# Kernel tuning notes

Measured on AMD Instinct MI355X. Metric: run time of the kernel, lower is better.

The kernel has to match this reference:

```python
import jax, jax.numpy as jnp
import numpy as np

U = 100000   # num_users
I = 50000    # num_items
N = U + I    # total nodes
D = 64       # embed_size
L = 3        # n_layers
E = 2000000  # num edges
EPS = 1e-12  # F.normalize default eps


def setup_inputs() -> dict:
    key = jax.random.key(0)
    k1, k2, k3, k4 = jax.random.split(key, 4)
    user_emb = jax.random.normal(k1, (U, D), dtype=jnp.float32) * 0.1
    item_emb = jax.random.normal(k2, (I, D), dtype=jnp.float32) * 0.1
    rows = jax.random.randint(k3, (E,), 0, N, dtype=jnp.int32)
    cols = jax.random.randint(k4, (E,), 0, N, dtype=jnp.int32)
    return {"user_emb": user_emb, "item_emb": item_emb, "rows": rows, "cols": cols}


def _spmm(vals, rows, cols, x):
    # sparse [N,N] @ dense [N,D] via gather + segment reduce
    return jax.ops.segment_sum(vals[:, None] * x[cols], rows, num_segments=N)


def _l2norm(x):
    return x / jnp.maximum(jnp.linalg.norm(x, axis=1, keepdims=True), EPS)


def reference(user_emb, item_emb, rows, cols):
    emb0 = jnp.concatenate([user_emb, item_emb], axis=0)  # [N, D]

    # laplacian_adj: G = D^-1/2 A D^-1/2 on the same edge set
    deg = jax.ops.segment_sum(jnp.ones((E,), emb0.dtype), rows, num_segments=N)
    d_is = jnp.where(deg > 0, deg ** -0.5, 0.0)
    g_vals = d_is[rows] * d_is[cols]  # [E]

    cur = emb0
    acc = emb0
    user_fine, item_fine = [], []
    for _ in range(L):
        gnn = _spmm(g_vals, rows, cols, cur)  # [N, D]
        # fine_laplacian_adj: cosine-sim edge scores, row-normalized
        gr = _l2norm(gnn[rows])
        gc = _l2norm(gnn[cols])
        scores = (jnp.sum(gr * gc, axis=1) + 1.0) * 0.5  # [E] in [0,1]
        rowsum = jax.ops.segment_sum(scores, rows, num_segments=N)
        d_inv = jnp.where(rowsum > 0, 1.0 / rowsum, 0.0)
        fine = _spmm(d_inv[rows] * scores, rows, cols, cur)  # [N, D]
        cur = gnn + fine
        acc = acc + cur
        user_fine.append(fine[:U])
        item_fine.append(fine[U:])

    u_embs = acc[:U]
    i_embs = acc[U:]
    return (u_embs, i_embs, jnp.stack(user_fine, 0), jnp.stack(item_fine, 0))
```

## Files before the change

### kernel.cpp

```cpp
#include <hip/hip_runtime.h>

namespace {

typedef unsigned short u16;
typedef __attribute__((__ext_vector_type__(2))) float f32x2;
typedef __attribute__((__ext_vector_type__(4))) float f32x4;

constexpr int Un = 100000;
constexpr int In = 50000;
constexpr int Nn = 150000;
constexpr int D  = 64;
constexpr int Ln = 3;
constexpr int En = 2000000;
constexpr int CHUNK = 1024;
constexpr int NB = (Nn + CHUNK - 1) / CHUNK;
constexpr int DSTR = 8;

__device__ __forceinline__ u16 f2bf(float f) {
    unsigned u = __float_as_uint(f);
    unsigned r = (u + 0x7FFFu + ((u >> 16) & 1u)) >> 16;
    return (u16)r;
}
__device__ __forceinline__ float bflo(unsigned u) {
    return __uint_as_float(u << 16);
}
__device__ __forceinline__ float bfhi(unsigned u) {
    return __uint_as_float(u & 0xFFFF0000u);
}
__device__ __forceinline__ unsigned pack2(float lo, float hi) {
    return (unsigned)f2bf(lo) | ((unsigned)f2bf(hi) << 16);
}

__device__ __forceinline__ f32x2 pkfma(f32x2 a, f32x2 b, f32x2 c) {
    f32x2 d;
    asm("v_pk_fma_f32 %0, %1, %2, %3" : "=v"(d) : "v"(a), "v"(b), "v"(c));
    return d;
}
__device__ __forceinline__ f32x2 pkadd(f32x2 a, f32x2 b) {
    f32x2 d;
    asm("v_pk_add_f32 %0, %1, %2" : "=v"(d) : "v"(a), "v"(b));
    return d;
}

__device__ __forceinline__ float dpp_add8(float x) {
    x += __uint_as_float((unsigned)__builtin_amdgcn_update_dpp(
        0, (int)__float_as_uint(x), 0xB1, 0xF, 0xF, true));
    x += __uint_as_float((unsigned)__builtin_amdgcn_update_dpp(
        0, (int)__float_as_uint(x), 0x4E, 0xF, 0xF, true));
    x += __uint_as_float((unsigned)__builtin_amdgcn_update_dpp(
        0, (int)__float_as_uint(x), 0x141, 0xF, 0xF, true));
    return x;
}

__device__ __forceinline__ void unp8(uint4 q, f32x2* o) {
    o[0].x = bflo(q.x); o[0].y = bfhi(q.x);
    o[1].x = bflo(q.y); o[1].y = bfhi(q.y);
    o[2].x = bflo(q.z); o[2].y = bfhi(q.z);
    o[3].x = bflo(q.w); o[3].y = bfhi(q.w);
}

__global__ void count_kernel(const int* __restrict__ rows, int* __restrict__ deg8,
                             int* __restrict__ eoff) {
    int e = blockIdx.x * blockDim.x + threadIdx.x;
    if (e < En) eoff[e] = atomicAdd(&deg8[(size_t)rows[e] * DSTR], 1);
}

__global__ void scan_partial(const int* __restrict__ deg8, float* __restrict__ d_is,
                             int* __restrict__ bsum) {
    int tid = threadIdx.x;
    int base = blockIdx.x * CHUNK + tid * 4;
    int s = 0;
#pragma unroll
    for (int i = 0; i < 4; ++i) {
        int idx = base + i;
        if (idx < Nn) {
            int d = deg8[(size_t)idx * DSTR];
            s += d;
            d_is[idx] = d > 0 ? rsqrtf((float)d) : 0.f;
        }
    }
    __shared__ int sh[256];
    sh[tid] = s;
    __syncthreads();
    for (int o = 128; o > 0; o >>= 1) {
        if (tid < o) sh[tid] += sh[tid + o];
        __syncthreads();
    }
    if (tid == 0) bsum[blockIdx.x] = sh[0];
}

__global__ void scan_top(int* __restrict__ bsum, int* __restrict__ row_ptr) {
    __shared__ int sh[256];
    int tid = threadIdx.x;
    int v = (tid < NB) ? bsum[tid] : 0;
    sh[tid] = v;
    __syncthreads();
    for (int o = 1; o < 256; o <<= 1) {
        int t = (tid >= o) ? sh[tid - o] : 0;
        __syncthreads();
        sh[tid] += t;
        __syncthreads();
    }
    if (tid < NB) bsum[tid] = sh[tid] - v;
    if (tid == 255) row_ptr[Nn] = sh[255];
}

__global__ void scan_final(const int* __restrict__ deg8, const int* __restrict__ bsum,
                           int* __restrict__ row_ptr) {
    int tid = threadIdx.x;
    int base = blockIdx.x * CHUNK + tid * 4;
    int v[4];
    int ts = 0;
#pragma unroll
    for (int i = 0; i < 4; ++i) {
        int idx = base + i;
        v[i] = (idx < Nn) ? deg8[(size_t)idx * DSTR] : 0;
        ts += v[i];
    }
    __shared__ int sh[256];
    sh[tid] = ts;
    __syncthreads();
    for (int o = 1; o < 256; o <<= 1) {
        int t = (tid >= o) ? sh[tid - o] : 0;
        __syncthreads();
        sh[tid] += t;
        __syncthreads();
    }
    int excl = bsum[blockIdx.x] + sh[tid] - ts;
#pragma unroll
    for (int i = 0; i < 4; ++i) {
        int idx = base + i;
        if (idx < Nn) row_ptr[idx] = excl;
        excl += v[i];
    }
}

__global__ void fill_kernel(const int* __restrict__ rows, const int* __restrict__ cols,
                            const int* __restrict__ row_ptr, const int* __restrict__ eoff,
                            int* __restrict__ col_off) {
    int e = blockIdx.x * blockDim.x + threadIdx.x;
    if (e >= En) return;
    col_off[row_ptr[rows[e]] + eoff[e]] = cols[e] << 7;
}

__global__ void init_kernel(const float* __restrict__ ue, const float* __restrict__ ie,
                            const float* __restrict__ d_is,
                            u16* __restrict__ cur, u16* __restrict__ S) {
    int i8 = (blockIdx.x * 256 + threadIdx.x) * 8;
    if (i8 >= Nn * D) return;
    const float* src = (i8 < Un * D) ? (ue + i8) : (ie + (i8 - Un * D));
    float4 v0 = ((const float4*)src)[0];
    float4 v1 = ((const float4*)src)[1];
    uint4 qc;
    qc.x = pack2(v0.x, v0.y); qc.y = pack2(v0.z, v0.w);
    qc.z = pack2(v1.x, v1.y); qc.w = pack2(v1.z, v1.w);
    *(uint4*)((char*)cur + (size_t)i8 * 2) = qc;
    float ds = d_is[i8 >> 6];
    uint4 qs;
    qs.x = pack2(v0.x * ds, v0.y * ds); qs.y = pack2(v0.z * ds, v0.w * ds);
    qs.z = pack2(v1.x * ds, v1.y * ds); qs.w = pack2(v1.z * ds, v1.w * ds);
    *(uint4*)((char*)S + (size_t)i8 * 2) = qs;
}

__global__ __launch_bounds__(256) void spmm_gnn(const u16* __restrict__ S_,
                                                u16* __restrict__ Qn_,
                                                const int* __restrict__ row_ptr,
                                                const int* __restrict__ col_off,
                                                const float* __restrict__ d_is,
                                                float* __restrict__ normv) {
    int r = (blockIdx.x * 256 + threadIdx.x) >> 6;
    if (r >= Nn) return;
    int lane = threadIdx.x & 63;
    int g = lane >> 3, l = lane & 7;
    unsigned l16 = (unsigned)l * 16u;
    const char* pS = (const char*)S_;
    int s = row_ptr[r], t = row_ptr[r + 1];
    float dr = d_is[r];
    f32x2 z; z.x = 0.f; z.y = 0.f;
    f32x2 a2[4] = {z, z, z, z};
    int deg = t - s;
    int nfull = deg >> 3;
    int rem = deg & 7;
    int jb = s + g;
#pragma unroll 2
    for (int i = 0; i < nfull; ++i) {
        unsigned off = (unsigned)col_off[jb + i * 8];
        uint4 q = *(const uint4*)(pS + (off + l16));
        f32x2 x2[4];
        unp8(q, x2);
#pragma unroll
        for (int p = 0; p < 4; ++p) a2[p] = pkadd(a2[p], x2[p]);
    }
    if (g < rem) {
        unsigned off = (unsigned)col_off[jb + nfull * 8];
        uint4 q = *(const uint4*)(pS + (off + l16));
        f32x2 x2[4];
        unp8(q, x2);
#pragma unroll
        for (int p = 0; p < 4; ++p) a2[p] = pkadd(a2[p], x2[p]);
    }
    float a[8] = {a2[0].x, a2[0].y, a2[1].x, a2[1].y,
                  a2[2].x, a2[2].y, a2[3].x, a2[3].y};
#pragma unroll
    for (int k = 0; k < 8; ++k) {
        a[k] += __shfl_xor(a[k], 8);
        a[k] += __shfl_xor(a[k], 16);
        a[k] += __shfl_xor(a[k], 32);
    }
    float sq = 0.f;
#pragma unroll
    for (int k = 0; k < 8; ++k) sq = fmaf(a[k], a[k], sq);
    sq = dpp_add8(sq);
    float gn = dr * sqrtf(sq);
    float nrm = fmaxf(gn, 1e-12f);
    float scale = dr / nrm;
    if (lane == 8) normv[r] = nrm;
    if (g == 0) {
        unsigned ro = ((unsigned)r << 7) + l16;
        uint4 on;
        on.x = pack2(a[0] * scale, a[1] * scale);
        on.y = pack2(a[2] * scale, a[3] * scale);
        on.z = pack2(a[4] * scale, a[5] * scale);
        on.w = pack2(a[6] * scale, a[7] * scale);
        *(uint4*)((char*)Qn_ + ro) = on;
    }
}

__global__ __launch_bounds__(256) void score_fine_kernel(const u16* __restrict__ A_,
                                                         const u16* __restrict__ Qn_,
                                                         u16* __restrict__ C_,
                                                         u16* __restrict__ S_,
                                                         const float* __restrict__ normv,
                                                         const float* __restrict__ d_is,
                                                         const int* __restrict__ row_ptr,
                                                         const int* __restrict__ col_off,
                                                         float* __restrict__ out, int layer) {
    int r = (blockIdx.x * 256 + threadIdx.x) >> 6;
    if (r >= Nn) return;
    int lane = threadIdx.x & 63;
    int g = lane >> 3, l = lane & 7;
    unsigned l16 = (unsigned)l * 16u;
    const char* pQn = (const char*)Qn_;
    const char* pA  = (const char*)A_;
    int s = row_ptr[r], t = row_ptr[r + 1];
    float dsr = d_is[r];
    float nrm = normv[r];
    unsigned ro = ((unsigned)r << 7) + l16;
    uint4 qbn = *(const uint4*)(pQn + ro);
    f32x2 b2[4];
    unp8(qbn, b2);
    f32x2 z; z.x = 0.f; z.y = 0.f;
    f32x2 facc[4] = {z, z, z, z};
    float rowsum = 0.f;
    int deg = t - s;
    int nfull = deg >> 3;
    int rem = deg & 7;
    int jb = s + g;
#pragma unroll 2
    for (int i = 0; i < nfull; ++i) {
        unsigned off = (unsigned)col_off[jb + i * 8];
        unsigned vo = off + l16;
        uint4 qx = *(const uint4*)(pQn + vo);
        uint4 qy = *(const uint4*)(pA + vo);
        f32x2 x2[4];
        unp8(qx, x2);
        f32x2 d2 = pkfma(b2[0], x2[0], z);
        d2 = pkfma(b2[1], x2[1], d2);
        d2 = pkfma(b2[2], x2[2], d2);
        d2 = pkfma(b2[3], x2[3], d2);
        float d = dpp_add8(d2.x + d2.y);
        float sc = fmaf(d, 0.5f, 0.5f);
        rowsum += sc;
        f32x2 y2[4];
        unp8(qy, y2);
        f32x2 sc2; sc2.x = sc; sc2.y = sc;
#pragma unroll
        for (int p = 0; p < 4; ++p) facc[p] = pkfma(sc2, y2[p], facc[p]);
    }
    if (g < rem) {
        unsigned off = (unsigned)col_off[jb + nfull * 8];
        unsigned vo = off + l16;
        uint4 qx = *(const uint4*)(pQn + vo);
        uint4 qy = *(const uint4*)(pA + vo);
        f32x2 x2[4];
        unp8(qx, x2);
        f32x2 d2 = pkfma(b2[0], x2[0], z);
        d2 = pkfma(b2[1], x2[1], d2);
        d2 = pkfma(b2[2], x2[2], d2);
        d2 = pkfma(b2[3], x2[3], d2);
        float d = dpp_add8(d2.x + d2.y);
        float sc = fmaf(d, 0.5f, 0.5f);
        rowsum += sc;
        f32x2 y2[4];
        unp8(qy, y2);
        f32x2 sc2; sc2.x = sc; sc2.y = sc;
#pragma unroll
        for (int p = 0; p < 4; ++p) facc[p] = pkfma(sc2, y2[p], facc[p]);
    }
    float f[8] = {facc[0].x, facc[0].y, facc[1].x, facc[1].y,
                  facc[2].x, facc[2].y, facc[3].x, facc[3].y};
    rowsum += __shfl_xor(rowsum, 8);
    rowsum += __shfl_xor(rowsum, 16);
    rowsum += __shfl_xor(rowsum, 32);
#pragma unroll
    for (int k = 0; k < 8; ++k) {
        f[k] += __shfl_xor(f[k], 8);
        f[k] += __shfl_xor(f[k], 16);
        f[k] += __shfl_xor(f[k], 32);
    }
    float di = rowsum > 0.f ? 1.f / rowsum : 0.f;
#pragma unroll
    for (int k = 0; k < 8; ++k) f[k] *= di;
    float bb[8] = {b2[0].x, b2[0].y, b2[1].x, b2[1].y,
                   b2[2].x, b2[2].y, b2[3].x, b2[3].y};
    float cn[8];
#pragma unroll
    for (int k = 0; k < 8; ++k) cn[k] = fmaf(bb[k], nrm, f[k]);
    if (g == 0) {
        uint4 qn;
        qn.x = pack2(cn[0], cn[1]); qn.y = pack2(cn[2], cn[3]);
        qn.z = pack2(cn[4], cn[5]); qn.w = pack2(cn[6], cn[7]);
        *(uint4*)((char*)C_ + ro) = qn;
    }
    if (g == 1 && layer != Ln - 1) {
        uint4 qs;
        qs.x = pack2(cn[0] * dsr, cn[1] * dsr);
        qs.y = pack2(cn[2] * dsr, cn[3] * dsr);
        qs.z = pack2(cn[4] * dsr, cn[5] * dsr);
        qs.w = pack2(cn[6] * dsr, cn[7] * dsr);
        *(uint4*)((char*)S_ + ro) = qs;
    }
    if (g >= 2 && g <= 3) {
        size_t fo;
        if (r < Un)
            fo = (size_t)Nn * D + (size_t)layer * Un * D + (size_t)r * D + l * 8;
        else
            fo = (size_t)Nn * D + (size_t)Ln * Un * D + (size_t)layer * In * D
                 + (size_t)(r - Un) * D + l * 8;
        if (g == 2) {
            f32x4 f0; f0.x = f[0]; f0.y = f[1]; f0.z = f[2]; f0.w = f[3];
            __builtin_nontemporal_store(f0, (f32x4*)(out + fo));
        } else {
            f32x4 f1; f1.x = f[4]; f1.y = f[5]; f1.z = f[6]; f1.w = f[7];
            __builtin_nontemporal_store(f1, (f32x4*)(out + fo) + 1);
        }
    }
}

__global__ void final_sum(const float* __restrict__ ue, const float* __restrict__ ie,
                          const u16* __restrict__ c1, const u16* __restrict__ c2,
                          const u16* __restrict__ c3, float* __restrict__ out) {
    int i8 = (blockIdx.x * 256 + threadIdx.x) * 8;
    if (i8 >= Nn * D) return;
    const float* src = (i8 < Un * D) ? (ue + i8) : (ie + (i8 - Un * D));
    float4 v0 = ((const float4*)src)[0];
    float4 v1 = ((const float4*)src)[1];
    uint4 q1 = *(const uint4*)((const char*)c1 + (size_t)i8 * 2);
    uint4 q2 = *(const uint4*)((const char*)c2 + (size_t)i8 * 2);
    uint4 q3 = *(const uint4*)((const char*)c3 + (size_t)i8 * 2);
    float o[8] = {v0.x, v0.y, v0.z, v0.w, v1.x, v1.y, v1.z, v1.w};
    f32x2 t1[4], t2[4], t3[4];
    unp8(q1, t1); unp8(q2, t2); unp8(q3, t3);
#pragma unroll
    for (int p = 0; p < 4; ++p) {
        o[2 * p]     = ((o[2 * p]     + t1[p].x) + t2[p].x) + t3[p].x;
        o[2 * p + 1] = ((o[2 * p + 1] + t1[p].y) + t2[p].y) + t3[p].y;
    }
    float4 w0, w1;
    w0.x = o[0]; w0.y = o[1]; w0.z = o[2]; w0.w = o[3];
    w1.x = o[4]; w1.y = o[5]; w1.z = o[6]; w1.w = o[7];
    ((float4*)(out + i8))[0] = w0;
    ((float4*)(out + i8))[1] = w1;
}

}

extern "C" void kernel_launch(void* const* d_in, const int* in_sizes, int n_in,
                              void* d_out, int out_size, void* d_ws, size_t ws_size,
                              hipStream_t stream) {
    const float* user_emb = (const float*)d_in[0];
    const float* item_emb = (const float*)d_in[1];
    const int* rows = (const int*)d_in[2];
    const int* cols = (const int*)d_in[3];
    float* out = (float*)d_out;

    char* ws = (char*)d_ws;
    size_t off = 0;
    auto alloc = [&](size_t bytes) -> void* {
        void* p = ws + off;
        off += (bytes + 255) & ~size_t(255);
        return p;
    };
    u16*   bufA    = (u16*)  alloc((size_t)Nn * D * 2);
    u16*   bufB    = (u16*)  alloc((size_t)Nn * D * 2);
    u16*   bufC    = (u16*)  alloc((size_t)Nn * D * 2);
    u16*   Qn      = (u16*)  alloc((size_t)Nn * D * 2);
    u16*   S       = (u16*)  alloc((size_t)Nn * D * 2);
    int*   col_off = (int*)  alloc((size_t)(En + 8) * 4);
    int*   deg8    = (int*)  alloc((size_t)Nn * DSTR * 4);
    int*   row_ptr = (int*)  alloc((size_t)(Nn + 1) * 4);
    float* d_is    = (float*)alloc((size_t)Nn * 4);
    float* normv   = (float*)alloc((size_t)Nn * 4);
    int*   bsum    = (int*)  alloc(4096);
    int*   eoff    = (int*)Qn;
    (void)ws_size; (void)in_sizes; (void)n_in; (void)out_size;

    hipMemsetAsync(deg8, 0, (size_t)Nn * DSTR * 4, stream);

    const int EB = (En + 255) / 256;
    count_kernel<<<EB, 256, 0, stream>>>(rows, deg8, eoff);
    scan_partial<<<NB, 256, 0, stream>>>(deg8, d_is, bsum);
    scan_top<<<1, 256, 0, stream>>>(bsum, row_ptr);
    scan_final<<<NB, 256, 0, stream>>>(deg8, bsum, row_ptr);
    fill_kernel<<<EB, 256, 0, stream>>>(rows, cols, row_ptr, eoff, col_off);
    init_kernel<<<(Nn * D / 8 + 255) / 256, 256, 0, stream>>>(user_emb, item_emb, d_is,
                                                              bufA, S);

    const int RB = Nn / 4;
    u16* Pl[4] = {bufA, bufB, bufC, bufA};
    for (int l = 0; l < Ln; ++l) {
        spmm_gnn<<<RB, 256, 0, stream>>>(S, Qn, row_ptr, col_off, d_is, normv);
        score_fine_kernel<<<RB, 256, 0, stream>>>(Pl[l], Qn, Pl[l + 1], S, normv,
                                                  d_is, row_ptr, col_off, out, l);
    }
    final_sum<<<(Nn * D / 8 + 255) / 256, 256, 0, stream>>>(user_emb, item_emb,
                                                            bufB, bufC, bufA, out);
}
```

Measured before the change: 764.5 us.

## Store normalized GNN rows as fp8 and recompute gnn inside score kernel

The spmm_gnn kernel now writes the L2-normalized aggregated embeddings as packed fp8 (8 bytes per lane chunk) instead of bf16, and no longer writes the per-row norm. The score/fine kernel gathers these fp8 vectors for the cosine scores. It rebuilds the exact gnn row by accumulating d_is[col]*cur[col] alongside the fine accumulation, which replaces nrm*Qn. This cuts the bytes of the per-edge random gather and drops the normv buffer. In exchange it adds an extra per-edge d_is load and more FMAs and shuffles, and fp8 precision in the cosine similarities risks accuracy. The degree-counter padding stride is also raised from 8 to 32.

```diff
diff --git a/kernel.cpp b/kernel.cpp
--- a/kernel.cpp
+++ b/kernel.cpp
@@ -14,7 +14,7 @@
 constexpr int En = 2000000;
 constexpr int CHUNK = 1024;
 constexpr int NB = (Nn + CHUNK - 1) / CHUNK;
-constexpr int DSTR = 8;
+constexpr int DSTR = 32;
 
 __device__ __forceinline__ u16 f2bf(float f) {
     unsigned u = __float_as_uint(f);
@@ -57,6 +57,13 @@
     o[1].x = bflo(q.y); o[1].y = bfhi(q.y);
     o[2].x = bflo(q.z); o[2].y = bfhi(q.z);
     o[3].x = bflo(q.w); o[3].y = bfhi(q.w);
+}
+
+__device__ __forceinline__ void unp8_fp8(uint2 q, f32x2* o) {
+    o[0] = __builtin_amdgcn_cvt_pk_f32_fp8((int)q.x, false);
+    o[1] = __builtin_amdgcn_cvt_pk_f32_fp8((int)q.x, true);
+    o[2] = __builtin_amdgcn_cvt_pk_f32_fp8((int)q.y, false);
+    o[3] = __builtin_amdgcn_cvt_pk_f32_fp8((int)q.y, true);
 }
 
 __global__ void count_kernel(const int* __restrict__ rows, int* __restrict__ deg8,
@@ -163,11 +170,10 @@
 }
 
 __global__ __launch_bounds__(256) void spmm_gnn(const u16* __restrict__ S_,
-                                                u16* __restrict__ Qn_,
+                                                unsigned* __restrict__ Qn8_,
                                                 const int* __restrict__ row_ptr,
                                                 const int* __restrict__ col_off,
-                                                const float* __restrict__ d_is,
-                                                float* __restrict__ normv) {
+                                                const float* __restrict__ d_is) {
     int r = (blockIdx.x * 256 + threadIdx.x) >> 6;
     if (r >= Nn) return;
     int lane = threadIdx.x & 63;
@@ -211,26 +217,28 @@
 #pragma unroll
     for (int k = 0; k < 8; ++k) sq = fmaf(a[k], a[k], sq);
     sq = dpp_add8(sq);
-    float gn = dr * sqrtf(sq);
-    float nrm = fmaxf(gn, 1e-12f);
-    float scale = dr / nrm;
-    if (lane == 8) normv[r] = nrm;
     if (g == 0) {
-        unsigned ro = ((unsigned)r << 7) + l16;
-        uint4 on;
-        on.x = pack2(a[0] * scale, a[1] * scale);
-        on.y = pack2(a[2] * scale, a[3] * scale);
-        on.z = pack2(a[4] * scale, a[5] * scale);
-        on.w = pack2(a[6] * scale, a[7] * scale);
-        *(uint4*)((char*)Qn_ + ro) = on;
+        float gn = dr * sqrtf(sq);
+        float nrm = fmaxf(gn, 1e-12f);
+        float scale = dr / nrm;
+        unsigned w0 = 0, w1 = 0;
+        w0 = (unsigned)__builtin_amdgcn_cvt_pk_fp8_f32(a[0] * scale, a[1] * scale,
+                                                       (int)w0, false);
+        w0 = (unsigned)__builtin_amdgcn_cvt_pk_fp8_f32(a[2] * scale, a[3] * scale,
+                                                       (int)w0, true);
+        w1 = (unsigned)__builtin_amdgcn_cvt_pk_fp8_f32(a[4] * scale, a[5] * scale,
+                                                       (int)w1, false);
+        w1 = (unsigned)__builtin_amdgcn_cvt_pk_fp8_f32(a[6] * scale, a[7] * scale,
+                                                       (int)w1, true);
+        uint2 qo; qo.x = w0; qo.y = w1;
+        *(uint2*)((char*)Qn8_ + ((unsigned)r << 6) + (unsigned)l * 8u) = qo;
     }
 }
 
 __global__ __launch_bounds__(256) void score_fine_kernel(const u16* __restrict__ A_,
-                                                         const u16* __restrict__ Qn_,
+                                                         const unsigned* __restrict__ Qn8_,
                                                          u16* __restrict__ C_,
                                                          u16* __restrict__ S_,
-                                                         const float* __restrict__ normv,
                                                          const float* __restrict__ d_is,
                                                          const int* __restrict__ row_ptr,
                                                          const int* __restrict__ col_off,
@@ -240,17 +248,18 @@
     int lane = threadIdx.x & 63;
     int g = lane >> 3, l = lane & 7;
     unsigned l16 = (unsigned)l * 16u;
-    const char* pQn = (const char*)Qn_;
+    unsigned l8 = (unsigned)l * 8u;
+    const char* pQ8 = (const char*)Qn8_;
     const char* pA  = (const char*)A_;
+    const char* pd  = (const char*)d_is;
     int s = row_ptr[r], t = row_ptr[r + 1];
-    float dsr = d_is[r];
-    float nrm = normv[r];
-    unsigned ro = ((unsigned)r << 7) + l16;
-    uint4 qbn = *(const uint4*)(pQn + ro);
+    float dr = d_is[r];
+    uint2 qb8 = *(const uint2*)(pQ8 + ((unsigned)r << 6) + l8);
     f32x2 b2[4];
-    unp8(qbn, b2);
+    unp8_fp8(qb8, b2);
     f32x2 z; z.x = 0.f; z.y = 0.f;
     f32x2 facc[4] = {z, z, z, z};
+    f32x2 gacc[4] = {z, z, z, z};
     float rowsum = 0.f;
     int deg = t - s;
     int nfull = deg >> 3;
@@ -259,11 +268,11 @@
 #pragma unroll 2
     for (int i = 0; i < nfull; ++i) {
         unsigned off = (unsigned)col_off[jb + i * 8];
-        unsigned vo = off + l16;
-        uint4 qx = *(const uint4*)(pQn + vo);
-        uint4 qy = *(const uint4*)(pA + vo);
+        float dv = *(const float*)(pd + (off >> 5));
+        uint2 q8 = *(const uint2*)(pQ8 + ((off >> 1) + l8));
+        uint4 qy = *(const uint4*)(pA + (off + l16));
         f32x2 x2[4];
-        unp8(qx, x2);
+        unp8_fp8(q8, x2);
         f32x2 d2 = pkfma(b2[0], x2[0], z);
         d2 = pkfma(b2[1], x2[1], d2);
         d2 = pkfma(b2[2], x2[2], d2);
@@ -274,16 +283,20 @@
         f32x2 y2[4];
         unp8(qy, y2);
         f32x2 sc2; sc2.x = sc; sc2.y = sc;
-#pragma unroll
-        for (int p = 0; p < 4; ++p) facc[p] = pkfma(sc2, y2[p], facc[p]);
+        f32x2 dv2; dv2.x = dv; dv2.y = dv;
+#pragma unroll
+        for (int p = 0; p < 4; ++p) {
+            facc[p] = pkfma(sc2, y2[p], facc[p]);
+            gacc[p] = pkfma(dv2, y2[p], gacc[p]);
+        }
     }
     if (g < rem) {
         unsigned off = (unsigned)col_off[jb + nfull * 8];
-        unsigned vo = off + l16;
-        uint4 qx = *(const uint4*)(pQn + vo);
-        uint4 qy = *(const uint4*)(pA + vo);
+        float dv = *(const float*)(pd + (off >> 5));
+        uint2 q8 = *(const uint2*)(pQ8 + ((off >> 1) + l8));
+        uint4 qy = *(const uint4*)(pA + (off + l16));
         f32x2 x2[4];
-        unp8(qx, x2);
+        unp8_fp8(q8, x2);
         f32x2 d2 = pkfma(b2[0], x2[0], z);
         d2 = pkfma(b2[1], x2[1], d2);
         d2 = pkfma(b2[2], x2[2], d2);
@@ -294,11 +307,17 @@
         f32x2 y2[4];
         unp8(qy, y2);
         f32x2 sc2; sc2.x = sc; sc2.y = sc;
-#pragma unroll
-        for (int p = 0; p < 4; ++p) facc[p] = pkfma(sc2, y2[p], facc[p]);
+        f32x2 dv2; dv2.x = dv; dv2.y = dv;
+#pragma unroll
+        for (int p = 0; p < 4; ++p) {
+            facc[p] = pkfma(sc2, y2[p], facc[p]);
+            gacc[p] = pkfma(dv2, y2[p], gacc[p]);
+        }
     }
     float f[8] = {facc[0].x, facc[0].y, facc[1].x, facc[1].y,
                   facc[2].x, facc[2].y, facc[3].x, facc[3].y};
+    float a[8] = {gacc[0].x, gacc[0].y, gacc[1].x, gacc[1].y,
+                  gacc[2].x, gacc[2].y, gacc[3].x, gacc[3].y};
     rowsum += __shfl_xor(rowsum, 8);
     rowsum += __shfl_xor(rowsum, 16);
     rowsum += __shfl_xor(rowsum, 32);
@@ -307,15 +326,18 @@
         f[k] += __shfl_xor(f[k], 8);
         f[k] += __shfl_xor(f[k], 16);
         f[k] += __shfl_xor(f[k], 32);
+        a[k] += __shfl_xor(a[k], 8);
+        a[k] += __shfl_xor(a[k], 16);
+        a[k] += __shfl_xor(a[k], 32);
     }
     float di = rowsum > 0.f ? 1.f / rowsum : 0.f;
-#pragma unroll
-    for (int k = 0; k < 8; ++k) f[k] *= di;
-    float bb[8] = {b2[0].x, b2[0].y, b2[1].x, b2[1].y,
-                   b2[2].x, b2[2].y, b2[3].x, b2[3].y};
-    float cn[8];
-#pragma unroll
-    for (int k = 0; k < 8; ++k) cn[k] = fmaf(bb[k], nrm, f[k]);
+    float fn[8], cn[8];
+#pragma unroll
+    for (int k = 0; k < 8; ++k) {
+        fn[k] = f[k] * di;
+        cn[k] = fmaf(a[k], dr, fn[k]);
+    }
+    unsigned ro = ((unsigned)r << 7) + l16;
     if (g == 0) {
         uint4 qn;
         qn.x = pack2(cn[0], cn[1]); qn.y = pack2(cn[2], cn[3]);
@@ -324,10 +346,10 @@
     }
     if (g == 1 && layer != Ln - 1) {
         uint4 qs;
-        qs.x = pack2(cn[0] * dsr, cn[1] * dsr);
-        qs.y = pack2(cn[2] * dsr, cn[3] * dsr);
-        qs.z = pack2(cn[4] * dsr, cn[5] * dsr);
-        qs.w = pack2(cn[6] * dsr, cn[7] * dsr);
+        qs.x = pack2(cn[0] * dr, cn[1] * dr);
+        qs.y = pack2(cn[2] * dr, cn[3] * dr);
+        qs.z = pack2(cn[4] * dr, cn[5] * dr);
+        qs.w = pack2(cn[6] * dr, cn[7] * dr);
         *(uint4*)((char*)S_ + ro) = qs;
     }
     if (g >= 2 && g <= 3) {
@@ -338,10 +360,10 @@
             fo = (size_t)Nn * D + (size_t)Ln * Un * D + (size_t)layer * In * D
                  + (size_t)(r - Un) * D + l * 8;
         if (g == 2) {
-            f32x4 f0; f0.x = f[0]; f0.y = f[1]; f0.z = f[2]; f0.w = f[3];
+            f32x4 f0; f0.x = fn[0]; f0.y = fn[1]; f0.z = fn[2]; f0.w = fn[3];
             __builtin_nontemporal_store(f0, (f32x4*)(out + fo));
         } else {
-            f32x4 f1; f1.x = f[4]; f1.y = f[5]; f1.z = f[6]; f1.w = f[7];
+            f32x4 f1; f1.x = fn[4]; f1.y = fn[5]; f1.z = fn[6]; f1.w = fn[7];
             __builtin_nontemporal_store(f1, (f32x4*)(out + fo) + 1);
         }
     }
@@ -391,18 +413,17 @@
         off += (bytes + 255) & ~size_t(255);
         return p;
     };
-    u16*   bufA    = (u16*)  alloc((size_t)Nn * D * 2);
-    u16*   bufB    = (u16*)  alloc((size_t)Nn * D * 2);
-    u16*   bufC    = (u16*)  alloc((size_t)Nn * D * 2);
-    u16*   Qn      = (u16*)  alloc((size_t)Nn * D * 2);
-    u16*   S       = (u16*)  alloc((size_t)Nn * D * 2);
-    int*   col_off = (int*)  alloc((size_t)(En + 8) * 4);
-    int*   deg8    = (int*)  alloc((size_t)Nn * DSTR * 4);
-    int*   row_ptr = (int*)  alloc((size_t)(Nn + 1) * 4);
-    float* d_is    = (float*)alloc((size_t)Nn * 4);
-    float* normv   = (float*)alloc((size_t)Nn * 4);
-    int*   bsum    = (int*)  alloc(4096);
-    int*   eoff    = (int*)Qn;
+    u16*      bufA    = (u16*)     alloc((size_t)Nn * D * 2);
+    u16*      bufB    = (u16*)     alloc((size_t)Nn * D * 2);
+    u16*      bufC    = (u16*)     alloc((size_t)Nn * D * 2);
+    unsigned* Qn8     = (unsigned*)alloc((size_t)Nn * D);
+    u16*      S       = (u16*)     alloc((size_t)Nn * D * 2);
+    int*      col_off = (int*)     alloc((size_t)(En + 8) * 4);
+    int*      deg8    = (int*)     alloc((size_t)Nn * DSTR * 4);
+    int*      row_ptr = (int*)     alloc((size_t)(Nn + 1) * 4);
+    float*    d_is    = (float*)   alloc((size_t)Nn * 4);
+    int*      bsum    = (int*)     alloc(4096);
+    int*      eoff    = (int*)Qn8;
     (void)ws_size; (void)in_sizes; (void)n_in; (void)out_size;
 
     hipMemsetAsync(deg8, 0, (size_t)Nn * DSTR * 4, stream);
@@ -419,8 +440,8 @@
     const int RB = Nn / 4;
     u16* Pl[4] = {bufA, bufB, bufC, bufA};
     for (int l = 0; l < Ln; ++l) {
-        spmm_gnn<<<RB, 256, 0, stream>>>(S, Qn, row_ptr, col_off, d_is, normv);
-        score_fine_kernel<<<RB, 256, 0, stream>>>(Pl[l], Qn, Pl[l + 1], S, normv,
+        spmm_gnn<<<RB, 256, 0, stream>>>(S, Qn8, row_ptr, col_off, d_is);
+        score_fine_kernel<<<RB, 256, 0, stream>>>(Pl[l], Qn8, Pl[l + 1], S,
                                                   d_is, row_ptr, col_off, out, l);
     }
     final_sum<<<(Nn * D / 8 + 255) / 256, 256, 0, stream>>>(user_emb, item_emb,
```

Result: slower. 798.3 us (+4.4%).

## Drop pre-scaled S buffer; apply column degree scaling inside gnn SpMM

Applied to the files above, without the earlier changes.

Removes the separate S buffer (embedding pre-multiplied by d_is) and its writes in init and score_fine. The gnn SpMM instead gathers the unscaled current embedding and loads d_is[col] per edge, fusing the scale into a packed FMA. This avoids writing and rereading an N×D bf16 array each layer, at the cost of an extra scalar gather per edge. It also adds nontemporal loads for col_off, occupancy hints in launch_bounds, and raises the degree-count stride DSTR.

```diff
diff --git a/kernel.cpp b/kernel.cpp
--- a/kernel.cpp
+++ b/kernel.cpp
@@ -14,7 +14,7 @@
 constexpr int En = 2000000;
 constexpr int CHUNK = 1024;
 constexpr int NB = (Nn + CHUNK - 1) / CHUNK;
-constexpr int DSTR = 8;
+constexpr int DSTR = 32;
 
 __device__ __forceinline__ u16 f2bf(float f) {
     unsigned u = __float_as_uint(f);
@@ -34,11 +34,6 @@
 __device__ __forceinline__ f32x2 pkfma(f32x2 a, f32x2 b, f32x2 c) {
     f32x2 d;
     asm("v_pk_fma_f32 %0, %1, %2, %3" : "=v"(d) : "v"(a), "v"(b), "v"(c));
-    return d;
-}
-__device__ __forceinline__ f32x2 pkadd(f32x2 a, f32x2 b) {
-    f32x2 d;
-    asm("v_pk_add_f32 %0, %1, %2" : "=v"(d) : "v"(a), "v"(b));
     return d;
 }
 
@@ -144,8 +139,7 @@
 }
 
 __global__ void init_kernel(const float* __restrict__ ue, const float* __restrict__ ie,
-                            const float* __restrict__ d_is,
-                            u16* __restrict__ cur, u16* __restrict__ S) {
+                            u16* __restrict__ cur) {
     int i8 = (blockIdx.x * 256 + threadIdx.x) * 8;
     if (i8 >= Nn * D) return;
     const float* src = (i8 < Un * D) ? (ue + i8) : (ie + (i8 - Un * D));
@@ -155,25 +149,21 @@
     qc.x = pack2(v0.x, v0.y); qc.y = pack2(v0.z, v0.w);
     qc.z = pack2(v1.x, v1.y); qc.w = pack2(v1.z, v1.w);
     *(uint4*)((char*)cur + (size_t)i8 * 2) = qc;
-    float ds = d_is[i8 >> 6];
-    uint4 qs;
-    qs.x = pack2(v0.x * ds, v0.y * ds); qs.y = pack2(v0.z * ds, v0.w * ds);
-    qs.z = pack2(v1.x * ds, v1.y * ds); qs.w = pack2(v1.z * ds, v1.w * ds);
-    *(uint4*)((char*)S + (size_t)i8 * 2) = qs;
-}
-
-__global__ __launch_bounds__(256) void spmm_gnn(const u16* __restrict__ S_,
-                                                u16* __restrict__ Qn_,
-                                                const int* __restrict__ row_ptr,
-                                                const int* __restrict__ col_off,
-                                                const float* __restrict__ d_is,
-                                                float* __restrict__ normv) {
+}
+
+__global__ __launch_bounds__(256, 8) void spmm_gnn(const u16* __restrict__ A_,
+                                                   u16* __restrict__ Qn_,
+                                                   const int* __restrict__ row_ptr,
+                                                   const int* __restrict__ col_off,
+                                                   const float* __restrict__ d_is,
+                                                   float* __restrict__ normv) {
     int r = (blockIdx.x * 256 + threadIdx.x) >> 6;
     if (r >= Nn) return;
     int lane = threadIdx.x & 63;
     int g = lane >> 3, l = lane & 7;
     unsigned l16 = (unsigned)l * 16u;
-    const char* pS = (const char*)S_;
+    const char* pA = (const char*)A_;
+    const char* pd = (const char*)d_is;
     int s = row_ptr[r], t = row_ptr[r + 1];
     float dr = d_is[r];
     f32x2 z; z.x = 0.f; z.y = 0.f;
@@ -184,20 +174,24 @@
     int jb = s + g;
 #pragma unroll 2
     for (int i = 0; i < nfull; ++i) {
-        unsigned off = (unsigned)col_off[jb + i * 8];
-        uint4 q = *(const uint4*)(pS + (off + l16));
+        unsigned off = (unsigned)__builtin_nontemporal_load(&col_off[jb + i * 8]);
+        float dv = *(const float*)(pd + (off >> 5));
+        uint4 q = *(const uint4*)(pA + (off + l16));
         f32x2 x2[4];
         unp8(q, x2);
-#pragma unroll
-        for (int p = 0; p < 4; ++p) a2[p] = pkadd(a2[p], x2[p]);
+        f32x2 dv2; dv2.x = dv; dv2.y = dv;
+#pragma unroll
+        for (int p = 0; p < 4; ++p) a2[p] = pkfma(dv2, x2[p], a2[p]);
     }
     if (g < rem) {
-        unsigned off = (unsigned)col_off[jb + nfull * 8];
-        uint4 q = *(const uint4*)(pS + (off + l16));
+        unsigned off = (unsigned)__builtin_nontemporal_load(&col_off[jb + nfull * 8]);
+        float dv = *(const float*)(pd + (off >> 5));
+        uint4 q = *(const uint4*)(pA + (off + l16));
         f32x2 x2[4];
         unp8(q, x2);
-#pragma unroll
-        for (int p = 0; p < 4; ++p) a2[p] = pkadd(a2[p], x2[p]);
+        f32x2 dv2; dv2.x = dv; dv2.y = dv;
+#pragma unroll
+        for (int p = 0; p < 4; ++p) a2[p] = pkfma(dv2, x2[p], a2[p]);
     }
     float a[8] = {a2[0].x, a2[0].y, a2[1].x, a2[1].y,
                   a2[2].x, a2[2].y, a2[3].x, a2[3].y};
@@ -226,15 +220,14 @@
     }
 }
 
-__global__ __launch_bounds__(256) void score_fine_kernel(const u16* __restrict__ A_,
-                                                         const u16* __restrict__ Qn_,
-                                                         u16* __restrict__ C_,
-                                                         u16* __restrict__ S_,
-                                                         const float* __restrict__ normv,
-                                                         const float* __restrict__ d_is,
-                                                         const int* __restrict__ row_ptr,
-                                                         const int* __restrict__ col_off,
-                                                         float* __restrict__ out, int layer) {
+__global__ __launch_bounds__(256, 8) void score_fine_kernel(const u16* __restrict__ A_,
+                                                            const u16* __restrict__ Qn_,
+                                                            u16* __restrict__ C_,
+                                                            const float* __restrict__ normv,
+                                                            const int* __restrict__ row_ptr,
+                                                            const int* __restrict__ col_off,
+                                                            float* __restrict__ out,
+                                                            int layer) {
     int r = (blockIdx.x * 256 + threadIdx.x) >> 6;
     if (r >= Nn) return;
     int lane = threadIdx.x & 63;
@@ -243,7 +236,6 @@
     const char* pQn = (const char*)Qn_;
     const char* pA  = (const char*)A_;
     int s = row_ptr[r], t = row_ptr[r + 1];
-    float dsr = d_is[r];
     float nrm = normv[r];
     unsigned ro = ((unsigned)r << 7) + l16;
     uint4 qbn = *(const uint4*)(pQn + ro);
@@ -258,7 +250,7 @@
     int jb = s + g;
 #pragma unroll 2
     for (int i = 0; i < nfull; ++i) {
-        unsigned off = (unsigned)col_off[jb + i * 8];
+        unsigned off = (unsigned)__builtin_nontemporal_load(&col_off[jb + i * 8]);
         unsigned vo = off + l16;
         uint4 qx = *(const uint4*)(pQn + vo);
         uint4 qy = *(const uint4*)(pA + vo);
@@ -278,7 +270,7 @@
         for (int p = 0; p < 4; ++p) facc[p] = pkfma(sc2, y2[p], facc[p]);
     }
     if (g < rem) {
-        unsigned off = (unsigned)col_off[jb + nfull * 8];
+        unsigned off = (unsigned)__builtin_nontemporal_load(&col_off[jb + nfull * 8]);
         unsigned vo = off + l16;
         uint4 qx = *(const uint4*)(pQn + vo);
         uint4 qy = *(const uint4*)(pA + vo);
@@ -322,22 +314,14 @@
         qn.z = pack2(cn[4], cn[5]); qn.w = pack2(cn[6], cn[7]);
         *(uint4*)((char*)C_ + ro) = qn;
     }
-    if (g == 1 && layer != Ln - 1) {
-        uint4 qs;
-        qs.x = pack2(cn[0] * dsr, cn[1] * dsr);
-        qs.y = pack2(cn[2] * dsr, cn[3] * dsr);
-        qs.z = pack2(cn[4] * dsr, cn[5] * dsr);
-        qs.w = pack2(cn[6] * dsr, cn[7] * dsr);
-        *(uint4*)((char*)S_ + ro) = qs;
-    }
-    if (g >= 2 && g <= 3) {
+    if (g == 1 || g == 2) {
         size_t fo;
         if (r < Un)
             fo = (size_t)Nn * D + (size_t)layer * Un * D + (size_t)r * D + l * 8;
         else
             fo = (size_t)Nn * D + (size_t)Ln * Un * D + (size_t)layer * In * D
                  + (size_t)(r - Un) * D + l * 8;
-        if (g == 2) {
+        if (g == 1) {
             f32x4 f0; f0.x = f[0]; f0.y = f[1]; f0.z = f[2]; f0.w = f[3];
             __builtin_nontemporal_store(f0, (f32x4*)(out + fo));
         } else {
@@ -395,7 +379,6 @@
     u16*   bufB    = (u16*)  alloc((size_t)Nn * D * 2);
     u16*   bufC    = (u16*)  alloc((size_t)Nn * D * 2);
     u16*   Qn      = (u16*)  alloc((size_t)Nn * D * 2);
-    u16*   S       = (u16*)  alloc((size_t)Nn * D * 2);
     int*   col_off = (int*)  alloc((size_t)(En + 8) * 4);
     int*   deg8    = (int*)  alloc((size_t)Nn * DSTR * 4);
     int*   row_ptr = (int*)  alloc((size_t)(Nn + 1) * 4);
@@ -413,15 +396,14 @@
     scan_top<<<1, 256, 0, stream>>>(bsum, row_ptr);
     scan_final<<<NB, 256, 0, stream>>>(deg8, bsum, row_ptr);
     fill_kernel<<<EB, 256, 0, stream>>>(rows, cols, row_ptr, eoff, col_off);
-    init_kernel<<<(Nn * D / 8 + 255) / 256, 256, 0, stream>>>(user_emb, item_emb, d_is,
-                                                              bufA, S);
+    init_kernel<<<(Nn * D / 8 + 255) / 256, 256, 0, stream>>>(user_emb, item_emb, bufA);
 
     const int RB = Nn / 4;
     u16* Pl[4] = {bufA, bufB, bufC, bufA};
     for (int l = 0; l < Ln; ++l) {
-        spmm_gnn<<<RB, 256, 0, stream>>>(S, Qn, row_ptr, col_off, d_is, normv);
-        score_fine_kernel<<<RB, 256, 0, stream>>>(Pl[l], Qn, Pl[l + 1], S, normv,
-                                                  d_is, row_ptr, col_off, out, l);
+        spmm_gnn<<<RB, 256, 0, stream>>>(Pl[l], Qn, row_ptr, col_off, d_is, normv);
+        score_fine_kernel<<<RB, 256, 0, stream>>>(Pl[l], Qn, Pl[l + 1], normv,
+                                                  row_ptr, col_off, out, l);
     }
     final_sum<<<(Nn * D / 8 + 255) / 256, 256, 0, stream>>>(user_emb, item_emb,
                                                             bufB, bufC, bufA, out);
```

Measured after the change: 821.5 us. 1.07x slower.
